# Kernel tuning notes

Hardware: AMD Instinct MI355X
Metric: run time of the kernel (lower is better)

The kernel has to match this reference:

```python
import jax, jax.numpy as jnp
import numpy as np

N = 100000   # nodes
G = 256      # graphs
E = 120000   # edges per relation
IN = 162
HID = 128
R = 5
L = 2        # extra RGCN layers beyond the initial one


def setup_inputs() -> dict:
    key = jax.random.key(0)
    ks = jax.random.split(key, 24)
    s = 0.05
    inp = {
        "X": jax.random.normal(ks[0], (N, IN), jnp.float32),
        "batch": jnp.sort(jax.random.randint(ks[6], (N,), 0, G)),
    }
    for i in range(R):
        inp[f"edge_index{i+1}"] = jax.random.randint(ks[1 + i], (2, E), 0, N)
    # RGCN initial layer params
    inp["W0"] = jax.random.normal(ks[7], (R, IN, HID), jnp.float32) * s
    inp["root0"] = jax.random.normal(ks[8], (IN, HID), jnp.float32) * s
    inp["b0"] = jnp.zeros((HID,), jnp.float32)
    # stacked params for the L hidden RGCN layers
    inp["Wl"] = jax.random.normal(ks[9], (L, R, HID, HID), jnp.float32) * s
    inp["rootl"] = jax.random.normal(ks[10], (L, HID, HID), jnp.float32) * s
    inp["bl"] = jnp.zeros((L, HID), jnp.float32)
    # classification head
    inp["Wc1"] = jax.random.normal(ks[11], (HID, HID), jnp.float32) * s
    inp["bc1"] = jnp.zeros((HID,), jnp.float32)
    inp["Wc2"] = jax.random.normal(ks[12], (HID, HID), jnp.float32) * s
    inp["bc2"] = jnp.zeros((HID,), jnp.float32)
    inp["Wc3"] = jax.random.normal(ks[13], (HID, 1), jnp.float32) * s
    inp["bc3"] = jnp.zeros((1,), jnp.float32)
    return inp


def _seg_mean(msg, dst, num):
    # scatter-mean over destination nodes (PyG RGCNConv uses aggr='mean' per relation)
    s = jax.ops.segment_sum(msg, dst, num_segments=num)
    c = jax.ops.segment_sum(jnp.ones(msg.shape[0], msg.dtype), dst, num_segments=num)
    return s / jnp.maximum(c, 1.0)[:, None]


def _rgcn(x, W, root, b, src, dst):
    # src, dst: [R, E]; W: [R, d_in, d_out]
    msgs = jnp.einsum("ref,rfh->reh", x[src], W)          # [R, E, HID]
    agg = jax.vmap(_seg_mean, in_axes=(0, 0, None))(msgs, dst, N)  # [R, N, HID]
    return x @ root + b + agg.sum(0)


def reference(X, edge_index1, edge_index2, edge_index3, edge_index4, edge_index5,
              batch, W0, root0, b0, Wl, rootl, bl, Wc1, bc1, Wc2, bc2, Wc3, bc3):
    ei = jnp.stack([edge_index1, edge_index2, edge_index3, edge_index4, edge_index5])  # [R,2,E]
    src, dst = ei[:, 0, :], ei[:, 1, :]
    h = jax.nn.relu(_rgcn(X, W0, root0, b0, src, dst))
    for l in range(L):
        h = jax.nn.relu(_rgcn(h, Wl[l], rootl[l], bl[l], src, dst))
    # mean readout over graphs
    s = jax.ops.segment_sum(h, batch, num_segments=G)
    c = jax.ops.segment_sum(jnp.ones((N,), h.dtype), batch, num_segments=G)
    read = s / jnp.maximum(c, 1.0)[:, None]
    h = jax.nn.relu(read @ Wc1 + bc1)
    h = jax.nn.relu(h @ Wc2 + bc2)
    return h @ Wc3 + bc3
```

## Files before the change

### kernel.cpp

```cpp
#include <hip/hip_runtime.h>

#define N_NODES 100000
#define NPAD    100096
#define NTILES  782
#define G_GRAPHS 256
#define IN_F 162
#define HID 128
#define R_REL 5
#define L_LAYERS 2
#define M5 (R_REL * N_NODES)
#define KSEG0 192
#define KC0   (6 * KSEG0)
#define KC1   (6 * HID)

typedef __attribute__((ext_vector_type(8))) short bf16x8;
typedef __attribute__((ext_vector_type(4))) float f32x4;

__device__ __forceinline__ short f2bf(float f) {
    union { float f; unsigned u; } v; v.f = f;
    unsigned r = (v.u + 0x7fffu + ((v.u >> 16) & 1u)) >> 16;
    return (short)r;
}
__device__ __forceinline__ float bf2f(unsigned short u) {
    union { unsigned u; float f; } v; v.u = ((unsigned)u) << 16;
    return v.f;
}

__global__ void k_count(const int* e0, const int* e1, const int* e2,
                        const int* e3, const int* e4, int* cnt, int E) {
    int gid = blockIdx.x * 256 + threadIdx.x;
    if (gid >= R_REL * E) return;
    int r = gid / E, e = gid - r * E;
    const int* ei = (r == 0) ? e0 : (r == 1) ? e1 : (r == 2) ? e2 : (r == 3) ? e3 : e4;
    atomicAdd(&cnt[r * N_NODES + ei[E + e]], 1);
}

__global__ __launch_bounds__(256) void k_scan1(const int* __restrict__ cnt,
                                               int* __restrict__ off, int* __restrict__ bsum) {
    __shared__ int ts[256];
    int t = threadIdx.x;
    int base = blockIdx.x * 1024 + t * 4;
    int v[4];
    #pragma unroll
    for (int j = 0; j < 4; j++) v[j] = (base + j < M5) ? cnt[base + j] : 0;
    int tsum = v[0] + v[1] + v[2] + v[3];
    ts[t] = tsum; __syncthreads();
    for (int o = 1; o < 256; o <<= 1) {
        int x = (t >= o) ? ts[t - o] : 0;
        __syncthreads();
        ts[t] += x;
        __syncthreads();
    }
    if (t == 255) bsum[blockIdx.x] = ts[255];
    int run = ts[t] - tsum;
    #pragma unroll
    for (int j = 0; j < 4; j++) { if (base + j < M5) off[base + j] = run; run += v[j]; }
}

__global__ __launch_bounds__(512) void k_scan2(int* bsum, int nblk) {
    __shared__ int ts[512];
    int t = threadIdx.x;
    int v = (t < nblk) ? bsum[t] : 0;
    ts[t] = v; __syncthreads();
    for (int o = 1; o < 512; o <<= 1) {
        int x = (t >= o) ? ts[t - o] : 0;
        __syncthreads();
        ts[t] += x;
        __syncthreads();
    }
    if (t < nblk) bsum[t] = ts[t] - v;
}

__global__ void k_scan3(const int* __restrict__ off, const int* __restrict__ bsum,
                        int* __restrict__ mstart, int* __restrict__ mcur,
                        const int* __restrict__ cnt, float* __restrict__ invc) {
    int i = blockIdx.x * 256 + threadIdx.x;
    if (i >= M5) return;
    int o = off[i] + bsum[i >> 10];
    mstart[i] = o;
    mcur[i] = o;
    int c = cnt[i];
    invc[i] = 1.0f / (float)max(c, 1);
    if (i == M5 - 1) mstart[M5] = o + c;
}

__global__ void k_fill(const int* e0, const int* e1, const int* e2,
                       const int* e3, const int* e4, int* mcur,
                       int* __restrict__ mrec, int E) {
    int gid = blockIdx.x * 256 + threadIdx.x;
    if (gid >= R_REL * E) return;
    int r = gid / E, e = gid - r * E;
    const int* ei = (r == 0) ? e0 : (r == 1) ? e1 : (r == 2) ? e2 : (r == 3) ? e3 : e4;
    int src = ei[e], dst = ei[E + e];
    int pos = atomicAdd(&mcur[r * N_NODES + dst], 1);
    mrec[pos] = src;
}

__global__ void k_castX(const float* __restrict__ X, unsigned short* __restrict__ Xb) {
    int gid = blockIdx.x * 256 + threadIdx.x;
    if (gid >= NPAD * KSEG0) return;
    int row = gid / KSEG0, k = gid - row * KSEG0;
    float v = (row < N_NODES && k < IN_F) ? X[(size_t)row * IN_F + k] : 0.f;
    Xb[gid] = (unsigned short)f2bf(v);
}

__global__ void k_tw0(const float* __restrict__ root0, const float* __restrict__ W0,
                      short* __restrict__ out) {
    int gid = blockIdx.x * 256 + threadIdx.x;
    if (gid >= 128 * KC0) return;
    int col = gid / KC0;
    int kk = gid - col * KC0;
    int chunk = kk / KSEG0, k = kk - chunk * KSEG0;
    float v = 0.f;
    if (k < IN_F)
        v = (chunk == 0) ? root0[k * HID + col]
                         : W0[((size_t)(chunk - 1) * IN_F + k) * HID + col];
    out[gid] = f2bf(v);
}

__global__ void k_twl(const float* __restrict__ rootl, const float* __restrict__ Wl,
                      short* __restrict__ out) {
    int gid = blockIdx.x * 256 + threadIdx.x;
    if (gid >= L_LAYERS * 128 * KC1) return;
    int l = gid / (128 * KC1);
    int rem = gid - l * 128 * KC1;
    int col = rem / KC1;
    int kk = rem - col * KC1;
    int chunk = kk / HID, k = kk - chunk * HID;
    float v = (chunk == 0) ? rootl[((size_t)l * HID + k) * HID + col]
                           : Wl[(((size_t)l * R_REL + (chunk - 1)) * HID + k) * HID + col];
    out[gid] = f2bf(v);
}

template<int KSEG>
__global__ __launch_bounds__(256)
void gemm_fused(const unsigned short* __restrict__ A0, const short* __restrict__ Wt,
                const float* __restrict__ bias,
                const int* __restrict__ mstart, const int* __restrict__ mrec,
                const float* __restrict__ invc,
                unsigned short* __restrict__ Hout) {
    constexpr int KS = KSEG / 32;
    constexpr int KCAT = 6 * KSEG;
    constexpr int SA = (KSEG == 192) ? 184 : 136;
    constexpr int NP = KSEG / 64;
    constexpr int EBUF = 512;
    __shared__ short Zs[128 * SA + 16];
    __shared__ int   sMS[5 * 129];
    __shared__ float sMW[5 * 128];
    __shared__ int   sE[EBUF];

    const int row0 = blockIdx.x * 128;
    const int tid = threadIdx.x;
    const int lane = tid & 63, wv = tid >> 6;
    const int quad = lane >> 4, l16 = lane & 15;
    const int wr0 = (wv >> 1) * 64, wc0 = (wv & 1) * 64;
    const int local0 = wv * 32 + quad * 8;

    for (int i = tid; i < 5 * 129; i += 256) {
        int seg = i / 129, o = i - seg * 129;
        sMS[i] = mstart[seg * N_NODES + min(row0 + o, N_NODES)];
    }
    for (int i = tid; i < 5 * 128; i += 256) {
        int seg = i >> 7, o = i & 127;
        int d = row0 + o;
        sMW[i] = (d < N_NODES) ? invc[seg * N_NODES + d] : 0.f;
    }

    const unsigned short* a0p = A0 + (size_t)(row0 + wr0 + l16) * KSEG + quad * 8;
    const short* Bp = Wt + (size_t)(wc0 + l16) * KCAT + quad * 8;

    f32x4 acc[4][4];
    #pragma unroll
    for (int i = 0; i < 4; i++)
        #pragma unroll
        for (int j = 0; j < 4; j++) acc[i][j] = (f32x4){0.f, 0.f, 0.f, 0.f};

    bf16x8 ac[4], bc[4], an[4], bn[4];
    #pragma unroll
    for (int i = 0; i < 4; i++) {
        ac[i] = *(const bf16x8*)(a0p + (size_t)i * 16 * KSEG);
        bc[i] = *(const bf16x8*)(Bp + (size_t)i * 16 * KCAT);
    }
    #pragma unroll
    for (int t = 0; t < KS; t++) {
        if (t + 1 < KS) {
            #pragma unroll
            for (int i = 0; i < 4; i++) {
                an[i] = *(const bf16x8*)(a0p + (size_t)i * 16 * KSEG + (t + 1) * 32);
                bn[i] = *(const bf16x8*)(Bp + (size_t)i * 16 * KCAT + (t + 1) * 32);
            }
        }
        #pragma unroll
        for (int i = 0; i < 4; i++)
            #pragma unroll
            for (int j = 0; j < 4; j++)
                acc[i][j] = __builtin_amdgcn_mfma_f32_16x16x32_bf16(ac[i], bc[j], acc[i][j], 0, 0, 0);
        if (t + 1 < KS) {
            #pragma unroll
            for (int i = 0; i < 4; i++) { ac[i] = an[i]; bc[i] = bn[i]; }
        }
    }
    __syncthreads();

    for (int sg = 0; sg < R_REL; sg++) {
        const int tb = (1 + sg) * KS;
        #pragma unroll
        for (int j = 0; j < 4; j++)
            bc[j] = *(const bf16x8*)(Bp + (size_t)j * 16 * KCAT + tb * 32);

        const int blo = sMS[sg * 129];
        {
            int cnt = sMS[sg * 129 + 128] - blo;
            if (cnt > EBUF) cnt = EBUF;
            for (int i = tid; i < cnt; i += 256) sE[i] = mrec[blo + i];
        }
        __syncthreads();

        {
            const int jlo = sMS[sg * 129 + local0];
            const int jhi = sMS[sg * 129 + local0 + 8];
            int di = 0;
            int nextb = sMS[sg * 129 + local0 + 1];
            float a0[NP], a1[NP], a2[NP], a3[NP];
            #pragma unroll
            for (int p = 0; p < NP; p++) { a0[p] = 0.f; a1[p] = 0.f; a2[p] = 0.f; a3[p] = 0.f; }
            uint2 v0[NP], v1[NP];
            if (jlo < jhi) {
                int jj = jlo - blo;
                int src = (jj < EBUF) ? sE[jj] : mrec[jlo];
                const unsigned short* r = A0 + (size_t)src * KSEG;
                #pragma unroll
                for (int p = 0; p < NP; p++) v0[p] = *(const uint2*)(r + p * 64 + l16 * 4);
            }
            if (jlo + 1 < jhi) {
                int jj = jlo + 1 - blo;
                int src = (jj < EBUF) ? sE[jj] : mrec[jlo + 1];
                const unsigned short* r = A0 + (size_t)src * KSEG;
                #pragma unroll
                for (int p = 0; p < NP; p++) v1[p] = *(const uint2*)(r + p * 64 + l16 * 4);
            }
            for (int j = jlo; ; j++) {
                while (di < 8 && j == nextb) {
                    float w = sMW[sg * 128 + local0 + di];
                    int zr = (local0 + di) * SA;
                    #pragma unroll
                    for (int p = 0; p < NP; p++) {
                        unsigned x = (unsigned)(unsigned short)f2bf(a0[p] * w) |
                                     ((unsigned)(unsigned short)f2bf(a1[p] * w) << 16);
                        unsigned y = (unsigned)(unsigned short)f2bf(a2[p] * w) |
                                     ((unsigned)(unsigned short)f2bf(a3[p] * w) << 16);
                        uint2 pv; pv.x = x; pv.y = y;
                        if (p < 2 || l16 < 10)
                            *(uint2*)&Zs[zr + p * 64 + l16 * 4] = pv;
                        a0[p] = 0.f; a1[p] = 0.f; a2[p] = 0.f; a3[p] = 0.f;
                    }
                    di++;
                    nextb = (di < 8) ? sMS[sg * 129 + local0 + di + 1] : 0x7fffffff;
                }
                if (j >= jhi) break;
                #pragma unroll
                for (int p = 0; p < NP; p++) {
                    a0[p] += bf2f((unsigned short)(v0[p].x & 0xffff));
                    a1[p] += bf2f((unsigned short)(v0[p].x >> 16));
                    a2[p] += bf2f((unsigned short)(v0[p].y & 0xffff));
                    a3[p] += bf2f((unsigned short)(v0[p].y >> 16));
                }
                #pragma unroll
                for (int p = 0; p < NP; p++) v0[p] = v1[p];
                if (j + 2 < jhi) {
                    int jj = j + 2 - blo;
                    int src = (jj < EBUF) ? sE[jj] : mrec[j + 2];
                    const unsigned short* r = A0 + (size_t)src * KSEG;
                    #pragma unroll
                    for (int p = 0; p < NP; p++) v1[p] = *(const uint2*)(r + p * 64 + l16 * 4);
                }
            }
        }
        __syncthreads();

        #pragma unroll
        for (int k = 0; k < KS; k++) {
            if (k + 1 < KS) {
                #pragma unroll
                for (int j = 0; j < 4; j++)
                    bn[j] = *(const bf16x8*)(Bp + (size_t)j * 16 * KCAT + (tb + k + 1) * 32);
            }
            #pragma unroll
            for (int i = 0; i < 4; i++)
                ac[i] = *(const bf16x8*)&Zs[(wr0 + i * 16 + l16) * SA + k * 32 + quad * 8];
            #pragma unroll
            for (int i = 0; i < 4; i++)
                #pragma unroll
                for (int j = 0; j < 4; j++)
                    acc[i][j] = __builtin_amdgcn_mfma_f32_16x16x32_bf16(ac[i], bc[j], acc[i][j], 0, 0, 0);
            if (k + 1 < KS) {
                #pragma unroll
                for (int j = 0; j < 4; j++) bc[j] = bn[j];
            }
        }
    }
    __syncthreads();

    float bj[4];
    #pragma unroll
    for (int j = 0; j < 4; j++) bj[j] = bias[wc0 + j * 16 + l16];
    #pragma unroll
    for (int i = 0; i < 4; i++)
        #pragma unroll
        for (int j = 0; j < 4; j++)
            #pragma unroll
            for (int reg = 0; reg < 4; reg++)
                Zs[(wr0 + i * 16 + quad * 4 + reg) * 136 + wc0 + j * 16 + l16] =
                    f2bf(fmaxf(acc[i][j][reg] + bj[j], 0.f));
    __syncthreads();

    #pragma unroll
    for (int s = 0; s < 8; s++) {
        int row = (tid >> 4) + s * 16;
        int col = (tid & 15) * 8;
        bf16x8 v = *(const bf16x8*)&Zs[row * 136 + col];
        *(bf16x8*)&Hout[(size_t)(row0 + row) * HID + col] = v;
    }
}

__global__ __launch_bounds__(128)
void k_pool(const unsigned short* __restrict__ h, const int* __restrict__ batch,
            float* __restrict__ pooled) {
    int c = threadIdx.x;
    int start = blockIdx.x * 128;
    if (start >= N_NODES) return;
    int end = min(start + 128, N_NODES);
    int g = batch[start];
    float s = 0.f;
    for (int i = start; i < end; i++) {
        int gi = batch[i];
        if (gi != g) { atomicAdd(&pooled[g * HID + c], s); s = 0.f; g = gi; }
        s += bf2f(h[(size_t)i * HID + c]);
    }
    atomicAdd(&pooled[g * HID + c], s);
}

__device__ int lower_bound_i(const int* a, int n, int v) {
    int lo = 0, hi = n;
    while (lo < hi) {
        int mid = (lo + hi) >> 1;
        if (a[mid] < v) lo = mid + 1; else hi = mid;
    }
    return lo;
}

__global__ __launch_bounds__(128)
void k_mlp(const float* __restrict__ pooled, const int* __restrict__ batch,
           const float* __restrict__ Wc1, const float* __restrict__ bc1,
           const float* __restrict__ Wc2, const float* __restrict__ bc2,
           const float* __restrict__ Wc3, const float* __restrict__ bc3,
           float* __restrict__ out) {
    int g = blockIdx.x;
    int c = threadIdx.x;
    __shared__ int range[2];
    if (c == 0) range[0] = lower_bound_i(batch, N_NODES, g);
    if (c == 1) range[1] = lower_bound_i(batch, N_NODES, g + 1);
    __syncthreads();
    float denom = fmaxf((float)(range[1] - range[0]), 1.0f);
    __shared__ float row[HID], h1[HID], h2[HID];
    row[c] = pooled[g * HID + c] / denom;
    __syncthreads();
    float acc = bc1[c];
    for (int k = 0; k < HID; k++) acc += row[k] * Wc1[k * HID + c];
    h1[c] = fmaxf(acc, 0.f);
    __syncthreads();
    acc = bc2[c];
    for (int k = 0; k < HID; k++) acc += h1[k] * Wc2[k * HID + c];
    h2[c] = fmaxf(acc, 0.f);
    __syncthreads();
    float t = h2[c] * Wc3[c];
    for (int off = 32; off > 0; off >>= 1) t += __shfl_down(t, off, 64);
    __shared__ float part[2];
    if ((c & 63) == 0) part[c >> 6] = t;
    __syncthreads();
    if (c == 0) out[g] = part[0] + part[1] + bc3[0];
}

extern "C" void kernel_launch(void* const* d_in, const int* in_sizes, int n_in,
                              void* d_out, int out_size, void* d_ws, size_t ws_size,
                              hipStream_t stream) {
    const float* X     = (const float*)d_in[0];
    const int*   batch = (const int*)d_in[1];
    const int*   e0 = (const int*)d_in[2];
    const int*   e1 = (const int*)d_in[3];
    const int*   e2 = (const int*)d_in[4];
    const int*   e3 = (const int*)d_in[5];
    const int*   e4 = (const int*)d_in[6];
    const float* W0    = (const float*)d_in[7];
    const float* root0 = (const float*)d_in[8];
    const float* b0    = (const float*)d_in[9];
    const float* Wl    = (const float*)d_in[10];
    const float* rootl = (const float*)d_in[11];
    const float* bl    = (const float*)d_in[12];
    const float* Wc1   = (const float*)d_in[13];
    const float* bc1   = (const float*)d_in[14];
    const float* Wc2   = (const float*)d_in[15];
    const float* bc2   = (const float*)d_in[16];
    const float* Wc3   = (const float*)d_in[17];
    const float* bc3   = (const float*)d_in[18];
    const int E = in_sizes[2] / 2;
    const int NE = R_REL * E;

    char* base = (char*)d_ws;
    size_t o = 0;
    auto carve = [&](size_t bytes) -> char* {
        char* p = base + o;
        o = (o + bytes + 255) & ~(size_t)255;
        return p;
    };
    unsigned short* h1 = (unsigned short*)carve((size_t)NPAD * HID * 2);
    unsigned short* Xb = (unsigned short*)carve((size_t)NPAD * KSEG0 * 2);
    int*   cnt    = (int*)carve((size_t)M5 * 4);
    float* invc   = (float*)carve((size_t)M5 * 4);
    int*   offsc  = (int*)carve((size_t)M5 * 4);
    int*   mstart = (int*)carve((size_t)(M5 + 1) * 4);
    int*   mrec   = (int*)carve((size_t)NE * 4);
    int*   bsum   = (int*)carve(2048);
    float* pooled = (float*)carve((size_t)G_GRAPHS * HID * 4);
    short* Wt0    = (short*)carve((size_t)128 * KC0 * 2);
    short* Wtl    = (short*)carve((size_t)L_LAYERS * 128 * KC1 * 2);
    int*   mcur   = offsc;
    unsigned short* h2 = Xb;

    hipMemsetAsync(cnt, 0, (size_t)M5 * 4, stream);
    hipMemsetAsync(pooled, 0, (size_t)G_GRAPHS * HID * 4, stream);
    int eg = (NE + 255) / 256;
    k_count<<<eg, 256, 0, stream>>>(e0, e1, e2, e3, e4, cnt, E);
    int nblk = (M5 + 1023) / 1024;
    k_scan1<<<nblk, 256, 0, stream>>>(cnt, offsc, bsum);
    k_scan2<<<1, 512, 0, stream>>>(bsum, nblk);
    k_scan3<<<(M5 + 255) / 256, 256, 0, stream>>>(offsc, bsum, mstart, mcur, cnt, invc);
    k_fill<<<eg, 256, 0, stream>>>(e0, e1, e2, e3, e4, mcur, mrec, E);
    k_castX<<<(NPAD * KSEG0 + 255) / 256, 256, 0, stream>>>(X, Xb);
    k_tw0<<<(128 * KC0 + 255) / 256, 256, 0, stream>>>(root0, W0, Wt0);
    k_twl<<<(L_LAYERS * 128 * KC1 + 255) / 256, 256, 0, stream>>>(rootl, Wl, Wtl);

    gemm_fused<KSEG0><<<NTILES, 256, 0, stream>>>(Xb, Wt0, b0, mstart, mrec, invc, h1);
    gemm_fused<HID><<<NTILES, 256, 0, stream>>>(h1, Wtl, bl, mstart, mrec, invc, h2);
    gemm_fused<HID><<<NTILES, 256, 0, stream>>>(h2, Wtl + (size_t)128 * KC1, bl + HID,
                                                mstart, mrec, invc, h1);

    k_pool<<<(N_NODES + 127) / 128, 128, 0, stream>>>(h1, batch, pooled);
    k_mlp<<<G_GRAPHS, 128, 0, stream>>>(pooled, batch, Wc1, bc1, Wc2, bc2, Wc3, bc3, (float*)d_out);
}
```

Baseline: 752.1 us.

## Double threads per fused RGCN tile and restructure gather to wide loads

Launches the fused gather+GEMM kernel with 512 threads instead of 256. Each wave now owns 32 rows of the MFMA tile rather than 64, and each 16-lane group aggregates 4 destination rows instead of 8, using 16-byte row loads plus an extra 8-byte load for the 192-wide input. The aim is more waves per tile to hide the latency of the irregular neighbor gathers. In exchange, each wave reloads the B operand for a smaller tile, the edge-index buffer in shared memory shrinks, and a barrier is added per relation. The padding columns of the first layer's LDS tile are also zeroed explicitly.

```diff
diff --git a/kernel.cpp b/kernel.cpp
--- a/kernel.cpp
+++ b/kernel.cpp
@@ -133,7 +133,7 @@
 }
 
 template<int KSEG>
-__global__ __launch_bounds__(256)
+__global__ __launch_bounds__(512)
 void gemm_fused(const unsigned short* __restrict__ A0, const short* __restrict__ Wt,
                 const float* __restrict__ bias,
                 const int* __restrict__ mstart, const int* __restrict__ mrec,
@@ -142,8 +142,7 @@
     constexpr int KS = KSEG / 32;
     constexpr int KCAT = 6 * KSEG;
     constexpr int SA = (KSEG == 192) ? 184 : 136;
-    constexpr int NP = KSEG / 64;
-    constexpr int EBUF = 512;
+    constexpr int EBUF = 320;
     __shared__ short Zs[128 * SA + 16];
     __shared__ int   sMS[5 * 129];
     __shared__ float sMW[5 * 128];
@@ -153,51 +152,57 @@
     const int tid = threadIdx.x;
     const int lane = tid & 63, wv = tid >> 6;
     const int quad = lane >> 4, l16 = lane & 15;
-    const int wr0 = (wv >> 1) * 64, wc0 = (wv & 1) * 64;
-    const int local0 = wv * 32 + quad * 8;
-
-    for (int i = tid; i < 5 * 129; i += 256) {
+    const int wr0 = (wv >> 1) * 32, wc0 = (wv & 1) * 64;
+    const int local0 = (tid >> 4) * 4;
+
+    for (int i = tid; i < 5 * 129; i += 512) {
         int seg = i / 129, o = i - seg * 129;
         sMS[i] = mstart[seg * N_NODES + min(row0 + o, N_NODES)];
     }
-    for (int i = tid; i < 5 * 128; i += 256) {
+    for (int i = tid; i < 5 * 128; i += 512) {
         int seg = i >> 7, o = i & 127;
         int d = row0 + o;
         sMW[i] = (d < N_NODES) ? invc[seg * N_NODES + d] : 0.f;
     }
+    if constexpr (KSEG == 192) {
+        for (int i = tid; i < 128 * 16; i += 512)
+            Zs[(i >> 4) * SA + 168 + (i & 15)] = 0;
+    }
 
     const unsigned short* a0p = A0 + (size_t)(row0 + wr0 + l16) * KSEG + quad * 8;
     const short* Bp = Wt + (size_t)(wc0 + l16) * KCAT + quad * 8;
 
-    f32x4 acc[4][4];
-    #pragma unroll
-    for (int i = 0; i < 4; i++)
+    f32x4 acc[2][4];
+    #pragma unroll
+    for (int i = 0; i < 2; i++)
         #pragma unroll
         for (int j = 0; j < 4; j++) acc[i][j] = (f32x4){0.f, 0.f, 0.f, 0.f};
 
-    bf16x8 ac[4], bc[4], an[4], bn[4];
-    #pragma unroll
-    for (int i = 0; i < 4; i++) {
-        ac[i] = *(const bf16x8*)(a0p + (size_t)i * 16 * KSEG);
-        bc[i] = *(const bf16x8*)(Bp + (size_t)i * 16 * KCAT);
-    }
+    bf16x8 ac[2], bc[4], an[2], bn[4];
+    #pragma unroll
+    for (int i = 0; i < 2; i++) ac[i] = *(const bf16x8*)(a0p + (size_t)i * 16 * KSEG);
+    #pragma unroll
+    for (int j = 0; j < 4; j++) bc[j] = *(const bf16x8*)(Bp + (size_t)j * 16 * KCAT);
     #pragma unroll
     for (int t = 0; t < KS; t++) {
         if (t + 1 < KS) {
             #pragma unroll
-            for (int i = 0; i < 4; i++) {
+            for (int i = 0; i < 2; i++)
                 an[i] = *(const bf16x8*)(a0p + (size_t)i * 16 * KSEG + (t + 1) * 32);
-                bn[i] = *(const bf16x8*)(Bp + (size_t)i * 16 * KCAT + (t + 1) * 32);
-            }
+            #pragma unroll
+            for (int j = 0; j < 4; j++)
+                bn[j] = *(const bf16x8*)(Bp + (size_t)j * 16 * KCAT + (t + 1) * 32);
         }
         #pragma unroll
-        for (int i = 0; i < 4; i++)
+        for (int i = 0; i < 2; i++)
             #pragma unroll
             for (int j = 0; j < 4; j++)
                 acc[i][j] = __builtin_amdgcn_mfma_f32_16x16x32_bf16(ac[i], bc[j], acc[i][j], 0, 0, 0);
         if (t + 1 < KS) {
             #pragma unroll
-            for (int i = 0; i < 4; i++) { ac[i] = an[i]; bc[i] = bn[i]; }
+            for (int i = 0; i < 2; i++) ac[i] = an[i];
+            #pragma unroll
+            for (int j = 0; j < 4; j++) bc[j] = bn[j];
         }
     }
     __syncthreads();
@@ -212,68 +217,86 @@
         {
             int cnt = sMS[sg * 129 + 128] - blo;
             if (cnt > EBUF) cnt = EBUF;
-            for (int i = tid; i < cnt; i += 256) sE[i] = mrec[blo + i];
+            for (int i = tid; i < cnt; i += 512) sE[i] = mrec[blo + i];
         }
         __syncthreads();
 
         {
             const int jlo = sMS[sg * 129 + local0];
-            const int jhi = sMS[sg * 129 + local0 + 8];
+            const int jhi = sMS[sg * 129 + local0 + 4];
             int di = 0;
             int nextb = sMS[sg * 129 + local0 + 1];
-            float a0[NP], a1[NP], a2[NP], a3[NP];
-            #pragma unroll
-            for (int p = 0; p < NP; p++) { a0[p] = 0.f; a1[p] = 0.f; a2[p] = 0.f; a3[p] = 0.f; }
-            uint2 v0[NP], v1[NP];
-            if (jlo < jhi) {
-                int jj = jlo - blo;
-                int src = (jj < EBUF) ? sE[jj] : mrec[jlo];
+            float a0 = 0.f, a1 = 0.f, a2 = 0.f, a3 = 0.f,
+                  a4 = 0.f, a5 = 0.f, a6 = 0.f, a7 = 0.f;
+            float e8 = 0.f, e9 = 0.f, e10 = 0.f, e11 = 0.f;
+            uint4 vA = {0, 0, 0, 0}, vB = {0, 0, 0, 0};
+            uint2 uA = {0, 0}, uB = {0, 0};
+
+            auto LD = [&](int j, uint4& v, uint2& u) {
+                int jj = j - blo;
+                int src = (jj < EBUF) ? sE[jj] : mrec[j];
                 const unsigned short* r = A0 + (size_t)src * KSEG;
-                #pragma unroll
-                for (int p = 0; p < NP; p++) v0[p] = *(const uint2*)(r + p * 64 + l16 * 4);
-            }
-            if (jlo + 1 < jhi) {
-                int jj = jlo + 1 - blo;
-                int src = (jj < EBUF) ? sE[jj] : mrec[jlo + 1];
-                const unsigned short* r = A0 + (size_t)src * KSEG;
-                #pragma unroll
-                for (int p = 0; p < NP; p++) v1[p] = *(const uint2*)(r + p * 64 + l16 * 4);
-            }
-            for (int j = jlo; ; j++) {
-                while (di < 8 && j == nextb) {
-                    float w = sMW[sg * 128 + local0 + di];
-                    int zr = (local0 + di) * SA;
-                    #pragma unroll
-                    for (int p = 0; p < NP; p++) {
-                        unsigned x = (unsigned)(unsigned short)f2bf(a0[p] * w) |
-                                     ((unsigned)(unsigned short)f2bf(a1[p] * w) << 16);
-                        unsigned y = (unsigned)(unsigned short)f2bf(a2[p] * w) |
-                                     ((unsigned)(unsigned short)f2bf(a3[p] * w) << 16);
-                        uint2 pv; pv.x = x; pv.y = y;
-                        if (p < 2 || l16 < 10)
-                            *(uint2*)&Zs[zr + p * 64 + l16 * 4] = pv;
-                        a0[p] = 0.f; a1[p] = 0.f; a2[p] = 0.f; a3[p] = 0.f;
+                v = *(const uint4*)(r + l16 * 8);
+                if constexpr (KSEG == 192) u = *(const uint2*)(r + 128 + l16 * 4);
+            };
+            auto CONSUME = [&](const uint4& v, const uint2& u) {
+                a0 += bf2f((unsigned short)(v.x & 0xffff));
+                a1 += bf2f((unsigned short)(v.x >> 16));
+                a2 += bf2f((unsigned short)(v.y & 0xffff));
+                a3 += bf2f((unsigned short)(v.y >> 16));
+                a4 += bf2f((unsigned short)(v.z & 0xffff));
+                a5 += bf2f((unsigned short)(v.z >> 16));
+                a6 += bf2f((unsigned short)(v.w & 0xffff));
+                a7 += bf2f((unsigned short)(v.w >> 16));
+                if constexpr (KSEG == 192) {
+                    e8  += bf2f((unsigned short)(u.x & 0xffff));
+                    e9  += bf2f((unsigned short)(u.x >> 16));
+                    e10 += bf2f((unsigned short)(u.y & 0xffff));
+                    e11 += bf2f((unsigned short)(u.y >> 16));
+                }
+            };
+            auto PK = [](float lo, float hi) {
+                return (unsigned)(unsigned short)f2bf(lo) |
+                       ((unsigned)(unsigned short)f2bf(hi) << 16);
+            };
+            auto FLUSH = [&]() {
+                float w = sMW[sg * 128 + local0 + di];
+                int zr = (local0 + di) * SA;
+                uint4 pv;
+                pv.x = PK(a0 * w, a1 * w); pv.y = PK(a2 * w, a3 * w);
+                pv.z = PK(a4 * w, a5 * w); pv.w = PK(a6 * w, a7 * w);
+                *(uint4*)&Zs[zr + l16 * 8] = pv;
+                if constexpr (KSEG == 192) {
+                    if (l16 < 10) {
+                        uint2 q; q.x = PK(e8 * w, e9 * w); q.y = PK(e10 * w, e11 * w);
+                        *(uint2*)&Zs[zr + 128 + l16 * 4] = q;
                     }
-                    di++;
-                    nextb = (di < 8) ? sMS[sg * 129 + local0 + di + 1] : 0x7fffffff;
+                    e8 = 0.f; e9 = 0.f; e10 = 0.f; e11 = 0.f;
+                }
+                a0 = 0.f; a1 = 0.f; a2 = 0.f; a3 = 0.f;
+                a4 = 0.f; a5 = 0.f; a6 = 0.f; a7 = 0.f;
+            };
+
+            if (jlo < jhi) LD(jlo, vA, uA);
+            if (jlo + 1 < jhi) LD(jlo + 1, vB, uB);
+            int j = jlo;
+            while (true) {
+                while (di < 4 && j == nextb) {
+                    FLUSH(); di++;
+                    nextb = (di < 4) ? sMS[sg * 129 + local0 + di + 1] : 0x7fffffff;
                 }
                 if (j >= jhi) break;
-                #pragma unroll
-                for (int p = 0; p < NP; p++) {
-                    a0[p] += bf2f((unsigned short)(v0[p].x & 0xffff));
-                    a1[p] += bf2f((unsigned short)(v0[p].x >> 16));
-                    a2[p] += bf2f((unsigned short)(v0[p].y & 0xffff));
-                    a3[p] += bf2f((unsigned short)(v0[p].y >> 16));
+                CONSUME(vA, uA);
+                if (j + 2 < jhi) LD(j + 2, vA, uA);
+                j++;
+                while (di < 4 && j == nextb) {
+                    FLUSH(); di++;
+                    nextb = (di < 4) ? sMS[sg * 129 + local0 + di + 1] : 0x7fffffff;
                 }
-                #pragma unroll
-                for (int p = 0; p < NP; p++) v0[p] = v1[p];
-                if (j + 2 < jhi) {
-                    int jj = j + 2 - blo;
-                    int src = (jj < EBUF) ? sE[jj] : mrec[j + 2];
-                    const unsigned short* r = A0 + (size_t)src * KSEG;
-                    #pragma unroll
-                    for (int p = 0; p < NP; p++) v1[p] = *(const uint2*)(r + p * 64 + l16 * 4);
-                }
+                if (j >= jhi) break;
+                CONSUME(vB, uB);
+                if (j + 2 < jhi) LD(j + 2, vB, uB);
+                j++;
             }
         }
         __syncthreads();
@@ -286,10 +309,10 @@
                     bn[j] = *(const bf16x8*)(Bp + (size_t)j * 16 * KCAT + (tb + k + 1) * 32);
             }
             #pragma unroll
-            for (int i = 0; i < 4; i++)
+            for (int i = 0; i < 2; i++)
                 ac[i] = *(const bf16x8*)&Zs[(wr0 + i * 16 + l16) * SA + k * 32 + quad * 8];
             #pragma unroll
-            for (int i = 0; i < 4; i++)
+            for (int i = 0; i < 2; i++)
                 #pragma unroll
                 for (int j = 0; j < 4; j++)
                     acc[i][j] = __builtin_amdgcn_mfma_f32_16x16x32_bf16(ac[i], bc[j], acc[i][j], 0, 0, 0);
@@ -298,14 +321,14 @@
                 for (int j = 0; j < 4; j++) bc[j] = bn[j];
             }
         }
-    }
-    __syncthreads();
+        __syncthreads();
+    }
 
     float bj[4];
     #pragma unroll
     for (int j = 0; j < 4; j++) bj[j] = bias[wc0 + j * 16 + l16];
     #pragma unroll
-    for (int i = 0; i < 4; i++)
+    for (int i = 0; i < 2; i++)
         #pragma unroll
         for (int j = 0; j < 4; j++)
             #pragma unroll
@@ -315,8 +338,8 @@
     __syncthreads();
 
     #pragma unroll
-    for (int s = 0; s < 8; s++) {
-        int row = (tid >> 4) + s * 16;
+    for (int s = 0; s < 4; s++) {
+        int row = (tid >> 4) + s * 32;
         int col = (tid & 15) * 8;
         bf16x8 v = *(const bf16x8*)&Zs[row * 136 + col];
         *(bf16x8*)&Hout[(size_t)(row0 + row) * HID + col] = v;
@@ -440,9 +463,9 @@
     k_tw0<<<(128 * KC0 + 255) / 256, 256, 0, stream>>>(root0, W0, Wt0);
     k_twl<<<(L_LAYERS * 128 * KC1 + 255) / 256, 256, 0, stream>>>(rootl, Wl, Wtl);
 
-    gemm_fused<KSEG0><<<NTILES, 256, 0, stream>>>(Xb, Wt0, b0, mstart, mrec, invc, h1);
-    gemm_fused<HID><<<NTILES, 256, 0, stream>>>(h1, Wtl, bl, mstart, mrec, invc, h2);
-    gemm_fused<HID><<<NTILES, 256, 0, stream>>>(h2, Wtl + (size_t)128 * KC1, bl + HID,
+    gemm_fused<KSEG0><<<NTILES, 512, 0, stream>>>(Xb, Wt0, b0, mstart, mrec, invc, h1);
+    gemm_fused<HID><<<NTILES, 512, 0, stream>>>(h1, Wtl, bl, mstart, mrec, invc, h2);
+    gemm_fused<HID><<<NTILES, 512, 0, stream>>>(h2, Wtl + (size_t)128 * KC1, bl + HID,
                                                 mstart, mrec, invc, h1);
 
     k_pool<<<(N_NODES + 127) / 128, 128, 0, stream>>>(h1, batch, pooled);
```

Result: slower. 896.0 us (+19.1%).

## Gather neighbor rows per wavefront with 8-deep batched loads instead of per-quad

Applied to the files above, without the earlier changes.

Restructures the per-relation neighbor aggregation so each whole wavefront handles 32 destination rows sequentially, with every lane owning two (or four) feature columns. Eight source-row loads are issued together before accumulating, which gives more memory-level parallelism and removes the per-quad imbalance in edge counts. It also zero-fills the padded LDS columns for the 162-wide layer, shrinks the edge index buffer, and moves the end-of-relation barrier inside the loop. The cost is longer serial chains per wave, extra clamped redundant loads in the tail batch, and more barriers.

```diff
diff --git a/kernel.cpp b/kernel.cpp
--- a/kernel.cpp
+++ b/kernel.cpp
@@ -142,8 +142,7 @@
     constexpr int KS = KSEG / 32;
     constexpr int KCAT = 6 * KSEG;
     constexpr int SA = (KSEG == 192) ? 184 : 136;
-    constexpr int NP = KSEG / 64;
-    constexpr int EBUF = 512;
+    constexpr int EBUF = 384;
     __shared__ short Zs[128 * SA + 16];
     __shared__ int   sMS[5 * 129];
     __shared__ float sMW[5 * 128];
@@ -154,7 +153,6 @@
     const int lane = tid & 63, wv = tid >> 6;
     const int quad = lane >> 4, l16 = lane & 15;
     const int wr0 = (wv >> 1) * 64, wc0 = (wv & 1) * 64;
-    const int local0 = wv * 32 + quad * 8;
 
     for (int i = tid; i < 5 * 129; i += 256) {
         int seg = i / 129, o = i - seg * 129;
@@ -164,6 +162,11 @@
         int seg = i >> 7, o = i & 127;
         int d = row0 + o;
         sMW[i] = (d < N_NODES) ? invc[seg * N_NODES + d] : 0.f;
+    }
+    if constexpr (KSEG == 192) {
+        for (int i = tid; i < 128 * 16; i += 256)
+            Zs[(i >> 4) * SA + 168 + (i & 15)] = 0;
+        if (tid < 16) Zs[128 * SA + tid] = 0;
     }
 
     const unsigned short* a0p = A0 + (size_t)(row0 + wr0 + l16) * KSEG + quad * 8;
@@ -217,64 +220,61 @@
         __syncthreads();
 
         {
-            const int jlo = sMS[sg * 129 + local0];
-            const int jhi = sMS[sg * 129 + local0 + 8];
+            const int mbase = sg * 129 + wv * 32;
+            const int jlo = sMS[mbase];
+            const int jhi = sMS[mbase + 32];
             int di = 0;
-            int nextb = sMS[sg * 129 + local0 + 1];
-            float a0[NP], a1[NP], a2[NP], a3[NP];
-            #pragma unroll
-            for (int p = 0; p < NP; p++) { a0[p] = 0.f; a1[p] = 0.f; a2[p] = 0.f; a3[p] = 0.f; }
-            uint2 v0[NP], v1[NP];
-            if (jlo < jhi) {
-                int jj = jlo - blo;
-                int src = (jj < EBUF) ? sE[jj] : mrec[jlo];
-                const unsigned short* r = A0 + (size_t)src * KSEG;
-                #pragma unroll
-                for (int p = 0; p < NP; p++) v0[p] = *(const uint2*)(r + p * 64 + l16 * 4);
+            int bnd = sMS[mbase + 1];
+            float s0 = 0.f, s1 = 0.f, s2 = 0.f, s3 = 0.f;
+            const int lx = (lane & 31) * 2;
+
+            auto FLUSH = [&]() {
+                float w = sMW[sg * 128 + wv * 32 + di];
+                int zr = (wv * 32 + di) * SA;
+                unsigned pv = (unsigned)(unsigned short)f2bf(s0 * w) |
+                              ((unsigned)(unsigned short)f2bf(s1 * w) << 16);
+                *(unsigned*)&Zs[zr + lane * 2] = pv;
+                if constexpr (KSEG == 192) {
+                    if (lane < 20) {
+                        unsigned qv = (unsigned)(unsigned short)f2bf(s2 * w) |
+                                      ((unsigned)(unsigned short)f2bf(s3 * w) << 16);
+                        *(unsigned*)&Zs[zr + 128 + lane * 2] = qv;
+                    }
+                }
+                s0 = 0.f; s1 = 0.f; s2 = 0.f; s3 = 0.f;
+            };
+
+            #define GLD(i, q, u) { \
+                int j_ = min(jb + i, jmax); int jj_ = j_ - blo; \
+                int src_ = (jj_ < EBUF) ? sE[jj_] : mrec[j_]; \
+                const unsigned short* r_ = A0 + (size_t)src_ * KSEG; \
+                q = *(const unsigned*)(r_ + lane * 2); \
+                if constexpr (KSEG == 192) u = *(const unsigned*)(r_ + 128 + lx); }
+
+            #define CNS(i, q, u) if (jb + i < jhi) { \
+                int j_ = jb + i; \
+                while (di < 32 && j_ == bnd) { \
+                    FLUSH(); di++; \
+                    bnd = (di < 32) ? sMS[mbase + di + 1] : 0x7fffffff; \
+                } \
+                s0 += bf2f((unsigned short)(q & 0xffff)); \
+                s1 += bf2f((unsigned short)(q >> 16)); \
+                if constexpr (KSEG == 192) { \
+                    s2 += bf2f((unsigned short)(u & 0xffff)); \
+                    s3 += bf2f((unsigned short)(u >> 16)); } }
+
+            for (int jb = jlo; jb < jhi; jb += 8) {
+                const int jmax = jhi - 1;
+                unsigned q0, q1, q2, q3, q4, q5, q6, q7;
+                unsigned u0 = 0, u1 = 0, u2 = 0, u3 = 0, u4 = 0, u5 = 0, u6 = 0, u7 = 0;
+                GLD(0, q0, u0) GLD(1, q1, u1) GLD(2, q2, u2) GLD(3, q3, u3)
+                GLD(4, q4, u4) GLD(5, q5, u5) GLD(6, q6, u6) GLD(7, q7, u7)
+                CNS(0, q0, u0) CNS(1, q1, u1) CNS(2, q2, u2) CNS(3, q3, u3)
+                CNS(4, q4, u4) CNS(5, q5, u5) CNS(6, q6, u6) CNS(7, q7, u7)
             }
-            if (jlo + 1 < jhi) {
-                int jj = jlo + 1 - blo;
-                int src = (jj < EBUF) ? sE[jj] : mrec[jlo + 1];
-                const unsigned short* r = A0 + (size_t)src * KSEG;
-                #pragma unroll
-                for (int p = 0; p < NP; p++) v1[p] = *(const uint2*)(r + p * 64 + l16 * 4);
-            }
-            for (int j = jlo; ; j++) {
-                while (di < 8 && j == nextb) {
-                    float w = sMW[sg * 128 + local0 + di];
-                    int zr = (local0 + di) * SA;
-                    #pragma unroll
-                    for (int p = 0; p < NP; p++) {
-                        unsigned x = (unsigned)(unsigned short)f2bf(a0[p] * w) |
-                                     ((unsigned)(unsigned short)f2bf(a1[p] * w) << 16);
-                        unsigned y = (unsigned)(unsigned short)f2bf(a2[p] * w) |
-                                     ((unsigned)(unsigned short)f2bf(a3[p] * w) << 16);
-                        uint2 pv; pv.x = x; pv.y = y;
-                        if (p < 2 || l16 < 10)
-                            *(uint2*)&Zs[zr + p * 64 + l16 * 4] = pv;
-                        a0[p] = 0.f; a1[p] = 0.f; a2[p] = 0.f; a3[p] = 0.f;
-                    }
-                    di++;
-                    nextb = (di < 8) ? sMS[sg * 129 + local0 + di + 1] : 0x7fffffff;
-                }
-                if (j >= jhi) break;
-                #pragma unroll
-                for (int p = 0; p < NP; p++) {
-                    a0[p] += bf2f((unsigned short)(v0[p].x & 0xffff));
-                    a1[p] += bf2f((unsigned short)(v0[p].x >> 16));
-                    a2[p] += bf2f((unsigned short)(v0[p].y & 0xffff));
-                    a3[p] += bf2f((unsigned short)(v0[p].y >> 16));
-                }
-                #pragma unroll
-                for (int p = 0; p < NP; p++) v0[p] = v1[p];
-                if (j + 2 < jhi) {
-                    int jj = j + 2 - blo;
-                    int src = (jj < EBUF) ? sE[jj] : mrec[j + 2];
-                    const unsigned short* r = A0 + (size_t)src * KSEG;
-                    #pragma unroll
-                    for (int p = 0; p < NP; p++) v1[p] = *(const uint2*)(r + p * 64 + l16 * 4);
-                }
-            }
+            while (di < 32) { FLUSH(); di++; }
+            #undef GLD
+            #undef CNS
         }
         __syncthreads();
 
@@ -298,8 +298,8 @@
                 for (int j = 0; j < 4; j++) bc[j] = bn[j];
             }
         }
-    }
-    __syncthreads();
+        __syncthreads();
+    }
 
     float bj[4];
     #pragma unroll
```

Result: faster. 726.9 us (-3.3%).
